# Performance work log

Hardware: AMD Instinct MI355X
Metric: run time of the kernel (lower is better)

The kernel has to match this reference:

```python
import jax, jax.numpy as jnp
import numpy as np

# ---- static skeleton topology (SMPL 24-joint kinematic tree) ----
J = 24
CIN = 32   # in_channels_per_joint
COUT = 32  # out_channels_per_joint
K = 3      # temporal kernel size
NEG_SLOPE = 0.2
ADJ_LIST = [[0,1,2,3],[1,0,4],[2,0,5],[3,0,6],[4,1,7],[5,2,8],[6,3,9],[7,4,10],[8,5,11],
            [9,6,12,13,14],[10,7],[11,8],[12,9,15],[13,9,16],[14,9,17],[15,12],[16,13,18],
            [17,14,19],[18,16,20],[19,17,21],[20,18,22],[21,19,23],[22,20],[23,21]]

# joint-level adjacency mask [J, J]
_mask_j = np.zeros((J, J), dtype=np.float32)
for i, nbrs in enumerate(ADJ_LIST):
    _mask_j[i, nbrs] = 1.0
# expand to channel-block mask [J*COUT, J*CIN, 1]
MASK = np.kron(_mask_j, np.ones((COUT, CIN), dtype=np.float32))[:, :, None]

# pooling: merge pairs of consecutive joints -> 12 regions of 2
REGIONS = np.arange(J).reshape(J // 2, 2)            # [12, 2]
R = REGIONS.shape[0]
# coarsened adjacency: region r ~ region s if any member joints are adjacent
POST_ADJ = (_mask_j.reshape(R, 2, R, 2).any(axis=(1, 3))).astype(np.int32)  # [12, 12]


def setup_inputs() -> dict:
    key = jax.random.key(0)
    k1, k2 = jax.random.split(key)
    B, T = 8, 4096
    x = jax.random.normal(k1, (B, J * CIN, T), dtype=jnp.float32)
    W = jax.random.normal(k2, (J * COUT, J * CIN, K), dtype=jnp.float32) * 0.02
    b = jnp.zeros((J * COUT,), dtype=jnp.float32)
    return {"x": x, "W": W, "b": b}


def reference(x, W, b):
    # SkeletalConv: adjacency-masked temporal conv1d (stride 1, SAME padding)
    Wm = W * jnp.asarray(MASK)
    y = jax.lax.conv_general_dilated(
        x, Wm, window_strides=(1,), padding="SAME",
        dimension_numbers=("NCW", "OIW", "NCW"))
    y = y + b[None, :, None]
    # LeakyReLU(0.2)
    y = jnp.where(y > 0, y, NEG_SLOPE * y)
    # SkeletalPooling: average channel blocks of joints within each region
    B, _, T = y.shape
    yr = y.reshape(B, J, COUT, T)              # [B, J, C, T]
    pooled = yr[:, jnp.asarray(REGIONS)]       # [B, R, 2, C, T]
    pooled = pooled.mean(axis=2).reshape(B, R * COUT, T)
    return pooled, jnp.asarray(REGIONS), jnp.asarray(POST_ADJ)
```

## Files before the change

kernel.cpp:

```cpp
#include <hip/hip_runtime.h>
#include <hip/hip_bf16.h>

#define J_     24
#define CIN_   32
#define COUT_  32
#define B_     8
#define T_     4096
#define R_     12
#define TT_    128
#define POOLED_SZ_ (B_ * R_ * COUT_ * T_)
#define XT_ELEMS_  ((size_t)B_ * T_ * (J_ * CIN_))
#define NFRAG_     420
#define PLROWS_    145
#define PLSTR_     (PLROWS_ * 16)
#define BSLAB_     (4 * PLSTR_)

typedef float  f32x4  __attribute__((ext_vector_type(4)));
typedef float  f32x16 __attribute__((ext_vector_type(16)));
typedef short  bf16x8 __attribute__((ext_vector_type(8)));
typedef unsigned short us8 __attribute__((ext_vector_type(8)));

__device__ __constant__ unsigned int ADJMASK[J_] = {
    0x0000000Fu, 0x00000013u, 0x00000025u, 0x00000049u, 0x00000092u, 0x00000124u,
    0x00000248u, 0x00000490u, 0x00000920u, 0x00007240u, 0x00000480u, 0x00000900u,
    0x00009200u, 0x00012200u, 0x00024200u, 0x00009000u, 0x00052000u, 0x000A4000u,
    0x00150000u, 0x002A0000u, 0x00540000u, 0x00A80000u, 0x00500000u, 0x00A00000u
};
__device__ __constant__ int ADJ_FLAT[70] = {
    0,1,2,3,  0,1,4,  0,2,5,  0,3,6,  1,4,7,  2,5,8,  3,6,9,  4,7,10,  5,8,11,
    6,9,12,13,14,  7,10,  8,11,  9,12,15,  9,13,16,  9,14,17,  12,15,
    13,16,18,  14,17,19,  16,18,20,  17,19,21,  18,20,22,  19,21,23,  20,22,  21,23
};
__device__ __constant__ int ADJ_OFF[J_ + 1] = {
    0,4,7,10,13,16,19,22,25,28,33,35,37,40,43,46,48,51,54,57,60,63,66,68,70
};
__device__ __constant__ int UNION_CNT[R_] = {5,5,6,6,8,4,5,5,6,6,6,4};
__device__ __constant__ int UNION_NB[R_][8] = {
    {0,1,2,3,4,0,0,0},      {0,2,3,5,6,0,0,0},      {1,2,4,5,7,8,0,0},
    {3,4,6,7,9,10,0,0},     {5,6,8,9,11,12,13,14},  {7,8,10,11,0,0,0,0},
    {9,12,13,15,16,0,0,0},  {9,12,14,15,17,0,0,0},  {13,14,16,17,18,19,0,0},
    {16,17,18,19,20,21,0,0},{18,19,20,21,22,23,0,0},{20,21,22,23,0,0,0,0}
};

static __device__ __forceinline__ unsigned short f2bf(float f) {
    unsigned u = __float_as_uint(f);
    unsigned r = (u + 0x7fffu + ((u >> 16) & 1u)) >> 16;
    return (unsigned short)r;
}

__global__ __launch_bounds__(256)
void skel_transpose(const float* __restrict__ x, unsigned short* __restrict__ xT)
{
    __shared__ float xs[32][257];
    const int tid = threadIdx.x;
    const int tt0 = blockIdx.x * 256;
    const int cg  = blockIdx.y;
    const int b   = blockIdx.z;

    const float* xp = x + ((size_t)b * (J_ * CIN_) + cg * 32) * T_ + tt0;
#pragma unroll
    for (int i = 0; i < 8; ++i) {
        const int idx = tid + i * 256;
        const int row = idx >> 6;
        const int c4  = (idx & 63) << 2;
        const float4 v = *(const float4*)(xp + (size_t)row * T_ + c4);
        xs[row][c4 + 0] = v.x; xs[row][c4 + 1] = v.y;
        xs[row][c4 + 2] = v.z; xs[row][c4 + 3] = v.w;
    }
    __syncthreads();

    union { unsigned short u[32]; uint4 q[4]; } pk;
#pragma unroll
    for (int c = 0; c < 32; ++c) pk.u[c] = f2bf(xs[c][tid]);
    unsigned short* dst = xT + ((size_t)b * T_ + tt0 + tid) * (J_ * CIN_) + cg * 32;
#pragma unroll
    for (int k = 0; k < 4; ++k) *(uint4*)(dst + k * 8) = pk.q[k];
}

__global__ __launch_bounds__(64)
void skel_pack(const float* __restrict__ W, unsigned short* __restrict__ wsW,
               float* __restrict__ out_regions, float* __restrict__ out_post)
{
    const int fb = blockIdx.x;
    const int l  = threadIdx.x;
    if (fb == NFRAG_) {
        for (int i = l; i < J_; i += 64) out_regions[i] = (float)i;
        for (int i = l; i < R_ * R_; i += 64) {
            const int r1 = i / R_, r2 = i - r1 * R_;
            const unsigned m = ADJMASK[2 * r1] | ADJMASK[2 * r1 + 1];
            out_post[i] = ((m >> (2 * r2)) & 3u) ? 1.0f : 0.0f;
        }
        return;
    }
    const int h   = fb & 1;
    const int tmp = fb >> 1;
    const int kw  = tmp % 3;
    const int e   = tmp / 3;
    int jout = 0;
    while (ADJ_OFF[jout + 1] <= e) ++jout;
    const int nb = ADJ_FLAT[e];
    const int co = l & 31;
    const int g2 = l >> 5;

    union { unsigned short u[8]; uint4 q; } pk;
#pragma unroll
    for (int j = 0; j < 8; ++j) {
        const int ci = h * 16 + g2 * 8 + j;
        const float w = W[((size_t)(jout * COUT_ + co) * (J_ * CIN_) + (nb * CIN_ + ci)) * 3 + kw];
        pk.u[j] = f2bf(w);
    }
    *(uint4*)(wsW + (size_t)fb * 512 + l * 8) = pk.q;
}

__global__ __launch_bounds__(512, 4)
void skel_main(const unsigned short* __restrict__ xT,
               const unsigned short* __restrict__ wsW,
               const float* __restrict__ bias, float* __restrict__ out)
{
    const int i    = blockIdx.x;
    const int xcd  = i & 7;
    const int slot = i >> 3;
    const int r    = slot % R_;
    const int gi   = slot / R_;
    const int g    = xcd + 8 * gi;
    const int b    = g >> 5;
    const int t0   = (g & 31) * TT_;

    const int tid  = threadIdx.x;
    const int wv   = tid >> 6;
    const int lane = tid & 63;
    const int l31  = lane & 31;
    const int g2   = lane >> 5;
    const int ws   = wv & 3;
    const int js   = wv >> 2;

    __shared__ __align__(16) unsigned char lds[8 * BSLAB_];
    unsigned char* ldsB = lds;

    {
        const int NU = UNION_CNT[r];
        if (wv < NU) {
            const int nb = UNION_NB[r][wv];
            const unsigned short* gb = xT + (size_t)b * T_ * (J_ * CIN_) + nb * CIN_;
            unsigned char* ldst = ldsB + wv * BSLAB_;
            const int p  = lane & 3;
            const int r0 = lane >> 2;
            us8 v[9];
#pragma unroll
            for (int L = 0; L < 9; ++L) {
                const int rt = L * 16 + r0;
                const int t  = t0 - 1 + rt;
                const int tc = t < 0 ? 0 : (t > T_ - 1 ? T_ - 1 : t);
                v[L] = *(const us8*)(gb + (size_t)tc * (J_ * CIN_) + p * 8);
                if ((unsigned)t >= (unsigned)T_) {
                    const us8 z = {0, 0, 0, 0, 0, 0, 0, 0};
                    v[L] = z;
                }
            }
#pragma unroll
            for (int L = 0; L < 9; ++L) {
                const int rt = L * 16 + r0;
                *(us8*)(ldst + p * PLSTR_ + rt * 16) = v[L];
            }
        }
    }
    __syncthreads();

    f32x16 acc;
#pragma unroll
    for (int q = 0; q < 16; ++q) acc[q] = 0.0f;

    const unsigned short* wsWl = wsW + lane * 8;
    const int rtb = ws * 32 + l31;
    const int jw  = 2 * r + js;
    const unsigned um = ADJMASK[2 * r] | ADJMASK[2 * r + 1];
    const int eBeg = ADJ_OFF[jw], eEnd = ADJ_OFF[jw + 1];

    for (int e = eBeg; e < eEnd; ++e) {
        const int nb   = ADJ_FLAT[e];
        const int slab = __popc(um & ((1u << nb) - 1u));
        const unsigned char*  bbase = ldsB + slab * BSLAB_;
        const unsigned short* ae    = wsWl + (size_t)e * 6 * 512;
#pragma unroll
        for (int kw = 0; kw < 3; ++kw) {
            const int rt = rtb + kw;
#pragma unroll
            for (int h = 0; h < 2; ++h) {
                const bf16x8 bv = *(const bf16x8*)(bbase + (2 * h + g2) * PLSTR_ + rt * 16);
                const bf16x8 a  = *(const bf16x8*)(ae + (size_t)(kw * 2 + h) * 512);
                acc = __builtin_amdgcn_mfma_f32_32x32x16_bf16(a, bv, acc, 0, 0, 0);
            }
        }
    }

    f32x4 yv[4];
#pragma unroll
    for (int qq = 0; qq < 4; ++qq) {
#pragma unroll
        for (int qi = 0; qi < 4; ++qi) {
            const int co = 8 * qq + 4 * g2 + qi;
            float y = acc[qq * 4 + qi] + bias[jw * COUT_ + co];
            yv[qq][qi] = (y > 0.f) ? y : 0.2f * y;
        }
    }

    __syncthreads();
    float* scr = (float*)lds;
    if (js == 1) {
#pragma unroll
        for (int qq = 0; qq < 4; ++qq)
            *(f32x4*)(scr + ws * 4096 + qq * 1024 + lane * 4) = yv[qq];
    }
    __syncthreads();
    if (js == 0) {
#pragma unroll
        for (int qq = 0; qq < 4; ++qq) {
            const f32x4 pv = *(const f32x4*)(scr + ws * 4096 + qq * 1024 + lane * 4);
#pragma unroll
            for (int qi = 0; qi < 4; ++qi) {
                const int co = 8 * qq + 4 * g2 + qi;
                out[((size_t)b * (R_ * COUT_) + r * COUT_ + co) * T_
                    + t0 + ws * 32 + l31] = 0.5f * (yv[qq][qi] + pv[qi]);
            }
        }
    }
}

extern "C" void kernel_launch(void* const* d_in, const int* in_sizes, int n_in,
                              void* d_out, int out_size, void* d_ws, size_t ws_size,
                              hipStream_t stream)
{
    const float* x    = (const float*)d_in[0];
    const float* W    = (const float*)d_in[1];
    const float* bias = (const float*)d_in[2];
    float* out = (float*)d_out;

    unsigned short* xT  = (unsigned short*)d_ws;
    unsigned short* wsW = xT + XT_ELEMS_;

    dim3 tgrid(T_ / 256, J_ * CIN_ / 32, B_);
    skel_transpose<<<tgrid, 256, 0, stream>>>(x, xT);

    float* out_regions = out + POOLED_SZ_;
    float* out_post    = out_regions + J_;
    skel_pack<<<NFRAG_ + 1, 64, 0, stream>>>(W, wsW, out_regions, out_post);

    skel_main<<<(T_ / TT_) * R_ * B_, 512, 0, stream>>>(xT, wsW, bias, out);
}
```

Before: 74.68 us.

## Fuse input transpose and bf16 conversion into main kernel's LDS staging

Removes the separate transpose kernel that wrote a bf16 time-major copy of x to workspace, and instead has the main kernel read fp32 x directly in channel-major rows, convert to bf16 and scatter into the LDS layout the MFMA loop expects. This cuts one kernel launch and a full write-plus-read round trip of the transposed activation buffer. In exchange, each block reads fp32 (twice the bytes), neighbouring blocks re-read overlapping joint channels, and the LDS writes become narrow 4-byte scattered stores.

```diff
diff --git a/kernel.cpp b/kernel.cpp
--- a/kernel.cpp
+++ b/kernel.cpp
@@ -9,7 +9,6 @@
 #define R_     12
 #define TT_    128
 #define POOLED_SZ_ (B_ * R_ * COUT_ * T_)
-#define XT_ELEMS_  ((size_t)B_ * T_ * (J_ * CIN_))
 #define NFRAG_     420
 #define PLROWS_    145
 #define PLSTR_     (PLROWS_ * 16)
@@ -46,35 +45,6 @@
     unsigned u = __float_as_uint(f);
     unsigned r = (u + 0x7fffu + ((u >> 16) & 1u)) >> 16;
     return (unsigned short)r;
-}
-
-__global__ __launch_bounds__(256)
-void skel_transpose(const float* __restrict__ x, unsigned short* __restrict__ xT)
-{
-    __shared__ float xs[32][257];
-    const int tid = threadIdx.x;
-    const int tt0 = blockIdx.x * 256;
-    const int cg  = blockIdx.y;
-    const int b   = blockIdx.z;
-
-    const float* xp = x + ((size_t)b * (J_ * CIN_) + cg * 32) * T_ + tt0;
-#pragma unroll
-    for (int i = 0; i < 8; ++i) {
-        const int idx = tid + i * 256;
-        const int row = idx >> 6;
-        const int c4  = (idx & 63) << 2;
-        const float4 v = *(const float4*)(xp + (size_t)row * T_ + c4);
-        xs[row][c4 + 0] = v.x; xs[row][c4 + 1] = v.y;
-        xs[row][c4 + 2] = v.z; xs[row][c4 + 3] = v.w;
-    }
-    __syncthreads();
-
-    union { unsigned short u[32]; uint4 q[4]; } pk;
-#pragma unroll
-    for (int c = 0; c < 32; ++c) pk.u[c] = f2bf(xs[c][tid]);
-    unsigned short* dst = xT + ((size_t)b * T_ + tt0 + tid) * (J_ * CIN_) + cg * 32;
-#pragma unroll
-    for (int k = 0; k < 4; ++k) *(uint4*)(dst + k * 8) = pk.q[k];
 }
 
 __global__ __launch_bounds__(64)
@@ -113,7 +83,7 @@
 }
 
 __global__ __launch_bounds__(512, 4)
-void skel_main(const unsigned short* __restrict__ xT,
+void skel_main(const float* __restrict__ x,
                const unsigned short* __restrict__ wsW,
                const float* __restrict__ bias, float* __restrict__ out)
 {
@@ -141,26 +111,37 @@
         const int NU = UNION_CNT[r];
         if (wv < NU) {
             const int nb = UNION_NB[r][wv];
-            const unsigned short* gb = xT + (size_t)b * T_ * (J_ * CIN_) + nb * CIN_;
+            const float* gx  = x + ((size_t)b * (J_ * CIN_) + nb * CIN_) * T_;
             unsigned char* ldst = ldsB + wv * BSLAB_;
-            const int p  = lane & 3;
-            const int r0 = lane >> 2;
-            us8 v[9];
-#pragma unroll
-            for (int L = 0; L < 9; ++L) {
-                const int rt = L * 16 + r0;
-                const int t  = t0 - 1 + rt;
-                const int tc = t < 0 ? 0 : (t > T_ - 1 ? T_ - 1 : t);
-                v[L] = *(const us8*)(gb + (size_t)tc * (J_ * CIN_) + p * 8);
-                if ((unsigned)t >= (unsigned)T_) {
-                    const us8 z = {0, 0, 0, 0, 0, 0, 0, 0};
-                    v[L] = z;
+            const int cp = lane & 15;
+            const int gq = lane >> 4;
+            const int tb = t0 - 4 + 32 * gq;
+            const float* rp0 = gx + (size_t)(2 * cp) * T_;
+            const float* rp1 = rp0 + T_;
+            unsigned char* wbase = ldst + (cp >> 2) * PLSTR_ + (cp & 3) * 4;
+#pragma unroll
+            for (int half = 0; half < 2; ++half) {
+                f32x4 v0[5], v1[5];
+#pragma unroll
+                for (int f = 0; f < 5; ++f) {
+                    int ta = tb + (half * 5 + f) * 4;
+                    ta = ta < 0 ? 0 : (ta > T_ - 4 ? T_ - 4 : ta);
+                    v0[f] = *(const f32x4*)(rp0 + ta);
+                    v1[f] = *(const f32x4*)(rp1 + ta);
                 }
-            }
-#pragma unroll
-            for (int L = 0; L < 9; ++L) {
-                const int rt = L * 16 + r0;
-                *(us8*)(ldst + p * PLSTR_ + rt * 16) = v[L];
+#pragma unroll
+                for (int k = 0; k < 17; ++k) {
+                    const int kk = half * 17 + k;
+                    const int li = 3 + kk - half * 20;
+                    const int rt = 32 * gq + kk;
+                    const int t  = t0 - 1 + rt;
+                    unsigned u = 0;
+                    if ((unsigned)t < (unsigned)T_) {
+                        u = (unsigned)f2bf(v0[li >> 2][li & 3])
+                          | ((unsigned)f2bf(v1[li >> 2][li & 3]) << 16);
+                    }
+                    *(unsigned*)(wbase + rt * 16) = u;
+                }
             }
         }
     }
@@ -235,15 +216,11 @@
     const float* bias = (const float*)d_in[2];
     float* out = (float*)d_out;
 
-    unsigned short* xT  = (unsigned short*)d_ws;
-    unsigned short* wsW = xT + XT_ELEMS_;
-
-    dim3 tgrid(T_ / 256, J_ * CIN_ / 32, B_);
-    skel_transpose<<<tgrid, 256, 0, stream>>>(x, xT);
+    unsigned short* wsW = (unsigned short*)d_ws;
 
     float* out_regions = out + POOLED_SZ_;
     float* out_post    = out_regions + J_;
     skel_pack<<<NFRAG_ + 1, 64, 0, stream>>>(W, wsW, out_regions, out_post);
 
-    skel_main<<<(T_ / TT_) * R_ * B_, 512, 0, stream>>>(xT, wsW, bias, out);
-}
+    skel_main<<<(T_ / TT_) * R_ * B_, 512, 0, stream>>>(x, wsW, bias, out);
+}
```

Result: slower. 89.70 us (+20.1%).
